# Kernel tuning notes

Hardware: AMD Instinct MI355X
Metric: run time of the kernel (lower is better)

## Reference

```python
import jax, jax.numpy as jnp
import numpy as np

C_S, C_P, FEAT_DIM, NUM_BINS = 256, 128, 64, 22
TOTAL_EDGE_FEATS = FEAT_DIM * 3 + NUM_BINS * 2  # 236
MAX_LEN = 2056


def get_index_embedding(indices, embed_size, max_len=MAX_LEN):
    # indices: [..., ] float; returns [..., embed_size]
    K = jnp.arange(embed_size // 2, dtype=jnp.float32)
    ang = indices[..., None] * jnp.pi / (max_len ** (2.0 * K / embed_size))
    return jnp.concatenate([jnp.sin(ang), jnp.cos(ang)], axis=-1)


def calc_distogram(pos, min_bin, max_bin, num_bins):
    # pos: [B, N, 3] -> one-hot distogram [B, N, N, num_bins]
    d = jnp.linalg.norm(pos[:, :, None, :] - pos[:, None, :, :], axis=-1)[..., None]
    lower = jnp.linspace(min_bin, max_bin, num_bins)
    upper = jnp.concatenate([lower[1:], jnp.array([1e8], dtype=jnp.float32)])
    return ((d > lower) & (d < upper)).astype(pos.dtype)


def layer_norm(x, gamma, beta, eps=1e-5):
    mu = jnp.mean(x, axis=-1, keepdims=True)
    var = jnp.mean((x - mu) ** 2, axis=-1, keepdims=True)
    return (x - mu) * jax.lax.rsqrt(var + eps) * gamma + beta


def setup_inputs() -> dict:
    key = jax.random.key(0)
    ks = jax.random.split(key, 12)
    B, N = 2, 512
    def lin(k, fan_in, shape):
        bound = 1.0 / np.sqrt(fan_in)
        return jax.random.uniform(k, shape, jnp.float32, -bound, bound)
    return {
        "s": jax.random.normal(ks[0], (B, N, C_S), jnp.float32),
        "t": jax.random.normal(ks[1], (B, N, 3), jnp.float32),
        "sc_t": jax.random.normal(ks[2], (B, N, 3), jnp.float32),
        "p_mask": jnp.ones((B, N, N), jnp.float32),
        "W_sp": lin(ks[3], C_S, (FEAT_DIM, C_S)),
        "b_sp": lin(ks[4], C_S, (FEAT_DIM,)),
        "W_rp": lin(ks[5], FEAT_DIM, (FEAT_DIM, FEAT_DIM)),
        "b_rp": lin(ks[5], FEAT_DIM, (FEAT_DIM,)),
        "W1": lin(ks[6], TOTAL_EDGE_FEATS, (C_P, TOTAL_EDGE_FEATS)),
        "b1": lin(ks[7], TOTAL_EDGE_FEATS, (C_P,)),
        "W2": lin(ks[8], C_P, (C_P, C_P)),
        "b2": lin(ks[9], C_P, (C_P,)),
        "W3": lin(ks[10], C_P, (C_P, C_P)),
        "b3": lin(ks[11], C_P, (C_P,)),
        "ln_g": jnp.ones((C_P,), jnp.float32),
        "ln_b": jnp.zeros((C_P,), jnp.float32),
    }


def reference(s, t, sc_t, p_mask, W_sp, b_sp, W_rp, b_rp, W1, b1, W2, b2, W3, b3, ln_g, ln_b):
    B, N, _ = s.shape
    # node embed then all-pairs broadcast-concat: [B,N,N,2*feat_dim]
    p_i = s @ W_sp.T + b_sp  # [B,N,feat_dim]
    cross = jnp.concatenate([
        jnp.broadcast_to(p_i[:, :, None, :], (B, N, N, FEAT_DIM)),
        jnp.broadcast_to(p_i[:, None, :, :], (B, N, N, FEAT_DIM)),
    ], axis=-1)
    # relative position embedding (res_idx=None -> arange)
    pos = jnp.broadcast_to(jnp.arange(N, dtype=jnp.float32)[None, :], (B, N))
    rel_pos = pos[:, :, None] - pos[:, None, :]
    pos_emb = get_index_embedding(rel_pos, FEAT_DIM)  # [B,N,N,feat_dim]
    relpos_feats = pos_emb @ W_rp.T + b_rp
    dist_feats = calc_distogram(t, 1e-3, 20.0, NUM_BINS)
    sc_feats = calc_distogram(sc_t, 1e-3, 20.0, NUM_BINS)
    all_edge = jnp.concatenate([cross, relpos_feats, dist_feats, sc_feats], axis=-1)
    h = jax.nn.relu(all_edge @ W1.T + b1)
    h = jax.nn.relu(h @ W2.T + b2)
    h = h @ W3.T + b3
    h = layer_norm(h, ln_g, ln_b)
    return h * p_mask[..., None]
```

## Files before the change

### kernel.cpp

```cpp
#include <hip/hip_runtime.h>

#define NN 512

typedef __attribute__((ext_vector_type(8))) short bf16x8;
typedef __attribute__((ext_vector_type(4))) float f32x4;

__device__ __forceinline__ unsigned short f2bf(float x) {
    union { float f; unsigned u; } c; c.f = x;
    unsigned u = c.u + 0x7fffu + ((c.u >> 16) & 1u);
    return (unsigned short)(u >> 16);
}

__device__ __forceinline__ float blo(unsigned u) {
    union { unsigned x; float f; } c; c.x = u << 16; return c.f;
}
__device__ __forceinline__ float bhi(unsigned u) {
    union { unsigned x; float f; } c; c.x = u & 0xffff0000u; return c.f;
}

__device__ __forceinline__ unsigned pk2(unsigned a, unsigned b, unsigned c,
                                        unsigned d, unsigned e) {
    float lo = blo(a) + blo(b) + blo(c) + blo(d) + blo(e);
    float hi = bhi(a) + bhi(b) + bhi(c) + bhi(d) + bhi(e);
    lo = fmaxf(lo, 0.0f);
    hi = fmaxf(hi, 0.0f);
    return (unsigned)f2bf(lo) | ((unsigned)f2bf(hi) << 16);
}

__device__ __forceinline__ int find_bin(float d) {
    int bin = 22;
    #pragma unroll
    for (int k = 0; k < 22; ++k) {
        float lo = (float)(1e-3 + k * ((20.0 - 1e-3) / 21.0));
        float hi = (k < 21) ? (float)(1e-3 + (k + 1) * ((20.0 - 1e-3) / 21.0)) : 1e8f;
        if (d > lo && d < hi) bin = k;
    }
    return bin;
}

__global__ __launch_bounds__(128) void k_prep(
        const float* __restrict__ s, const float* __restrict__ t,
        const float* __restrict__ sct,
        const float* __restrict__ Wsp, const float* __restrict__ bsp,
        const float* __restrict__ Wrp, const float* __restrict__ brp,
        const float* __restrict__ W1, const float* __restrict__ b1,
        const float* __restrict__ W2, const float* __restrict__ W3,
        float* __restrict__ p_i, unsigned short* __restrict__ relTb,
        unsigned short* __restrict__ WdTb, unsigned short* __restrict__ WscTb,
        unsigned short* __restrict__ w2a, unsigned short* __restrict__ w3a,
        unsigned short* __restrict__ binT)
{
    __shared__ float sh[2][256];
    const int blk = blockIdx.x, tid = threadIdx.x;

    if (blk < 23) {
        const int bin = blk, c = tid;
        WdTb[bin * 128 + c]  = (bin < 22) ? f2bf(W1[c * 236 + 192 + bin]) : (unsigned short)0;
        WscTb[bin * 128 + c] = (bin < 22) ? f2bf(W1[c * 236 + 214 + bin]) : (unsigned short)0;
    } else if (blk < 55) {
        const int seg = blk - 23;
        const int isW3 = seg >> 4;
        const int idx = (seg & 15) * 128 + tid;
        const int lane = idx & 63, ks = (idx >> 6) & 3, ct = idx >> 8;
        const float* W = isW3 ? W3 : W2;
        unsigned short* dst = isW3 ? w3a : w2a;
        const float* wp = W + (ct * 16 + (lane & 15)) * 128 + ks * 32 + (lane >> 4) * 8;
        unsigned r0 = (unsigned)f2bf(wp[0]) | ((unsigned)f2bf(wp[1]) << 16);
        unsigned r1 = (unsigned)f2bf(wp[2]) | ((unsigned)f2bf(wp[3]) << 16);
        unsigned r2 = (unsigned)f2bf(wp[4]) | ((unsigned)f2bf(wp[5]) << 16);
        unsigned r3 = (unsigned)f2bf(wp[6]) | ((unsigned)f2bf(wp[7]) << 16);
        uint4 v = { r0, r1, r2, r3 };
        *(uint4*)(dst + idx * 8) = v;
    } else if (blk < 1078) {
        const int row = blk - 55;
        const float d = (float)(row - 511);
        if (tid < 32) {
            float f = powf(2056.0f, (float)tid * (1.0f / 32.0f));
            float ang = d * 3.14159265358979323846f / f;
            sh[0][tid] = sinf(ang);
            sh[0][tid + 32] = cosf(ang);
        }
        __syncthreads();
        if (tid < 64) {
            const float* wr = Wrp + tid * 64;
            float a = brp[tid];
            #pragma unroll
            for (int k = 0; k < 64; ++k) a += sh[0][k] * wr[k];
            sh[1][tid] = a;
        }
        __syncthreads();
        const float* w = W1 + tid * 236 + 128;
        float a = b1[tid];
        #pragma unroll
        for (int k = 0; k < 64; ++k) a += sh[1][k] * w[k];
        relTb[row * 128 + tid] = f2bf(a);
    } else if (blk < 1590) {
        const int half = tid >> 6, ch = tid & 63;
        const int row = (blk - 1078) * 2 + half;
        *(float4*)&sh[half][ch * 4] = *(const float4*)&s[row * 256 + ch * 4];
        __syncthreads();
        const float* w = Wsp + ch * 256;
        float acc = bsp[ch];
        #pragma unroll 8
        for (int k = 0; k < 256; k += 4)
            acc += sh[half][k]*w[k] + sh[half][k+1]*w[k+1] + sh[half][k+2]*w[k+2] + sh[half][k+3]*w[k+3];
        p_i[row * 64 + ch] = acc;
    } else {
        const int pair = (blk - 1590) * 128 + tid;
        const int bi = pair >> 9, j = pair & (NN - 1);
        const int rj = (bi & ~(NN - 1)) + j;
        float ax = t[bi*3+0] - t[rj*3+0];
        float ay = t[bi*3+1] - t[rj*3+1];
        float az = t[bi*3+2] - t[rj*3+2];
        int bD = find_bin(sqrtf(ax*ax + ay*ay + az*az));
        float sx = sct[bi*3+0] - sct[rj*3+0];
        float sy = sct[bi*3+1] - sct[rj*3+1];
        float sz = sct[bi*3+2] - sct[rj*3+2];
        int bS = find_bin(sqrtf(sx*sx + sy*sy + sz*sz));
        binT[pair] = (unsigned short)(bD | (bS << 5));
    }
}

__global__ __launch_bounds__(128) void k_ql(const float* __restrict__ p_i,
        const float* __restrict__ W1,
        unsigned short* __restrict__ qLb, unsigned short* __restrict__ qRb)
{
    __shared__ float pr[64];
    const int row = blockIdx.x, tid = threadIdx.x;
    if (tid < 16) *(float4*)&pr[tid * 4] = *(const float4*)&p_i[row * 64 + tid * 4];
    __syncthreads();
    const float* w = W1 + tid * 236;
    float aL = 0.f, aR = 0.f;
    #pragma unroll
    for (int k = 0; k < 64; ++k) { aL += pr[k] * w[k]; aR += pr[k] * w[64 + k]; }
    qLb[row * 128 + tid] = f2bf(aL);
    qRb[row * 128 + tid] = f2bf(aR);
}

#define H1_OFF  0
#define H2_OFF  16384
#define LNP_OFF 32768
#define SMEM_SZ 37888

__global__ __launch_bounds__(512, 4) void k_main(
    const float* __restrict__ pmask,
    const unsigned short* __restrict__ qLb, const unsigned short* __restrict__ qRb,
    const unsigned short* __restrict__ relTb, const unsigned short* __restrict__ WdTb,
    const unsigned short* __restrict__ WscTb, const unsigned short* __restrict__ binT,
    const unsigned short* __restrict__ w2a, const unsigned short* __restrict__ w3a,
    const float* __restrict__ b2, const float* __restrict__ b3,
    const float* __restrict__ lng, const float* __restrict__ lnb,
    float* __restrict__ out)
{
    __shared__ __align__(16) char smem[SMEM_SZ];

    const int tid  = threadIdx.x;
    const int l    = tid & 63;
    const int w    = tid >> 6;
    const int jloc = l & 15;
    const int gq   = l >> 4;

    const int blk   = blockIdx.x;
    const int bi    = blk >> 3;
    const int i     = bi & (NN - 1);
    const int bbase = bi & ~(NN - 1);
    const int j0    = (blk & 7) * 64;

    bf16x8 w2r[4], w3r[4];
    #pragma unroll
    for (int ks = 0; ks < 4; ++ks) {
        w2r[ks] = *(const bf16x8*)(w2a + (w * 256 + ks * 64 + l) * 8);
        w3r[ks] = *(const bf16x8*)(w3a + (w * 256 + ks * 64 + l) * 8);
    }
    const int cch = w * 16 + gq * 4;
    const float4 b2f = *(const float4*)(b2 + cch);
    const float4 b3f = *(const float4*)(b3 + cch);
    const float4 g4  = *(const float4*)(lng + cch);
    const float4 be4 = *(const float4*)(lnb + cch);
    float maskv[4];
    #pragma unroll
    for (int tt = 0; tt < 4; ++tt)
        maskv[tt] = pmask[(size_t)bi * NN + j0 + tt * 16 + jloc];

    {
        const int r = tid >> 3, q = tid & 7;
        const unsigned bv = binT[bi * NN + j0 + r];
        const int bD = bv & 31, bS = (int)(bv >> 5);
        const unsigned short* qLp = qLb + (size_t)bi * 128;
        const unsigned short* qRp = qRb + (size_t)(bbase + j0 + r) * 128;
        const unsigned short* rTp = relTb + (size_t)(i - (j0 + r) + NN - 1) * 128;
        const unsigned short* dTp = WdTb + bD * 128;
        const unsigned short* sTp = WscTb + bS * 128;
        const int hswz = (r & 7) << 4;
        #pragma unroll
        for (int u = 0; u < 2; ++u) {
            const int c0 = q * 16 + u * 8;
            uint4 A = *(const uint4*)(qLp + c0);
            uint4 B = *(const uint4*)(qRp + c0);
            uint4 C = *(const uint4*)(rTp + c0);
            uint4 D = *(const uint4*)(dTp + c0);
            uint4 E = *(const uint4*)(sTp + c0);
            uint4 P;
            P.x = pk2(A.x, B.x, C.x, D.x, E.x);
            P.y = pk2(A.y, B.y, C.y, D.y, E.y);
            P.z = pk2(A.z, B.z, C.z, D.z, E.z);
            P.w = pk2(A.w, B.w, C.w, D.w, E.w);
            *(uint4*)(smem + H1_OFF + ((r * 256 + c0 * 2) ^ hswz)) = P;
        }
    }
    __syncthreads();

    const int rswz = (jloc & 7) << 4;

    #pragma unroll
    for (int tt = 0; tt < 4; ++tt) {
        const int rowb = (tt * 16 + jloc) * 256;
        f32x4 a2 = {0.f, 0.f, 0.f, 0.f};
        #pragma unroll
        for (int ks = 0; ks < 4; ++ks) {
            bf16x8 bfr = *(bf16x8*)(smem + H1_OFF + ((rowb + ks * 64 + gq * 16) ^ rswz));
            a2 = __builtin_amdgcn_mfma_f32_16x16x32_bf16(w2r[ks], bfr, a2, 0, 0, 0);
        }
        float y0 = fmaxf(a2[0] + b2f.x, 0.0f);
        float y1 = fmaxf(a2[1] + b2f.y, 0.0f);
        float y2 = fmaxf(a2[2] + b2f.z, 0.0f);
        float y3 = fmaxf(a2[3] + b2f.w, 0.0f);
        uint2 pk;
        pk.x = (unsigned)f2bf(y0) | ((unsigned)f2bf(y1) << 16);
        pk.y = (unsigned)f2bf(y2) | ((unsigned)f2bf(y3) << 16);
        *(uint2*)(smem + H2_OFF + ((rowb + cch * 2) ^ rswz)) = pk;
    }
    __syncthreads();

    f32x4 acc3[4];
    float* lnp = (float*)(smem + LNP_OFF);
    #pragma unroll
    for (int tt = 0; tt < 4; ++tt) {
        const int rowb = (tt * 16 + jloc) * 256;
        f32x4 a3 = {0.f, 0.f, 0.f, 0.f};
        #pragma unroll
        for (int ks = 0; ks < 4; ++ks) {
            bf16x8 bfr = *(bf16x8*)(smem + H2_OFF + ((rowb + ks * 64 + gq * 16) ^ rswz));
            a3 = __builtin_amdgcn_mfma_f32_16x16x32_bf16(w3r[ks], bfr, a3, 0, 0, 0);
        }
        a3[0] += b3f.x; a3[1] += b3f.y; a3[2] += b3f.z; a3[3] += b3f.w;
        acc3[tt] = a3;
        float s1 = a3[0] + a3[1] + a3[2] + a3[3];
        float s2 = a3[0]*a3[0] + a3[1]*a3[1] + a3[2]*a3[2] + a3[3]*a3[3];
        s1 += __shfl_xor(s1, 16); s2 += __shfl_xor(s2, 16);
        s1 += __shfl_xor(s1, 32); s2 += __shfl_xor(s2, 32);
        if (l < 16) {
            float2 p2 = make_float2(s1, s2);
            *(float2*)(lnp + (tt * 16 + jloc) * 20 + w * 2) = p2;
        }
    }
    __syncthreads();

    #pragma unroll
    for (int tt = 0; tt < 4; ++tt) {
        const int row = tt * 16 + jloc;
        float s1 = 0.f, s2 = 0.f;
        #pragma unroll
        for (int pp = 0; pp < 4; ++pp) {
            float4 v = *(float4*)(lnp + row * 20 + pp * 4);
            s1 += v.x + v.z; s2 += v.y + v.w;
        }
        const float mean = s1 * (1.0f / 128.0f);
        const float var  = s2 * (1.0f / 128.0f) - mean * mean;
        const float rstd = rsqrtf(var + 1e-5f);
        const float mk = maskv[tt];
        f32x4 a3 = acc3[tt];
        f32x4 o;
        o[0] = ((a3[0] - mean) * rstd * g4.x + be4.x) * mk;
        o[1] = ((a3[1] - mean) * rstd * g4.y + be4.y) * mk;
        o[2] = ((a3[2] - mean) * rstd * g4.z + be4.z) * mk;
        o[3] = ((a3[3] - mean) * rstd * g4.w + be4.w) * mk;
        const int slot = (w * 4 + gq) ^ (row & 31);
        *(f32x4*)(smem + row * 512 + slot * 16) = o;
    }
    __syncthreads();

    float* ob = out + ((size_t)(bi * NN + j0)) * 128;
    #pragma unroll
    for (int it = 0; it < 4; ++it) {
        const int boff = it * 8192 + tid * 16;
        const int row  = boff >> 9;
        const int slot = (boff >> 4) & 31;
        const int sslt = slot ^ (row & 31);
        f32x4 v = *(f32x4*)(smem + row * 512 + sslt * 16);
        __builtin_nontemporal_store(v, (f32x4*)(ob + (boff >> 2)));
    }
}

extern "C" void kernel_launch(void* const* d_in, const int* in_sizes, int n_in,
                              void* d_out, int out_size, void* d_ws, size_t ws_size,
                              hipStream_t stream)
{
    const float* s   = (const float*)d_in[0];
    const float* t   = (const float*)d_in[1];
    const float* sct = (const float*)d_in[2];
    const float* pm  = (const float*)d_in[3];
    const float* Wsp = (const float*)d_in[4];
    const float* bsp = (const float*)d_in[5];
    const float* Wrp = (const float*)d_in[6];
    const float* brp = (const float*)d_in[7];
    const float* W1  = (const float*)d_in[8];
    const float* b1  = (const float*)d_in[9];
    const float* W2  = (const float*)d_in[10];
    const float* b2  = (const float*)d_in[11];
    const float* W3  = (const float*)d_in[12];
    const float* b3  = (const float*)d_in[13];
    const float* lng = (const float*)d_in[14];
    const float* lnb = (const float*)d_in[15];

    float* ws = (float*)d_ws;
    float*          p_i   = ws;
    unsigned short* qLb   = (unsigned short*)(ws + 65536);
    unsigned short* qRb   = (unsigned short*)(ws + 131072);
    unsigned short* relTb = (unsigned short*)(ws + 196608);
    unsigned short* WdTb  = (unsigned short*)(ws + 262144);
    unsigned short* WscTb = (unsigned short*)(ws + 263616);
    unsigned short* w2a   = (unsigned short*)(ws + 265088);
    unsigned short* w3a   = (unsigned short*)(ws + 273280);
    unsigned short* binT  = (unsigned short*)(ws + 281472);

    k_prep<<<5686, 128, 0, stream>>>(s, t, sct, Wsp, bsp, Wrp, brp, W1, b1, W2, W3,
                                     p_i, relTb, WdTb, WscTb, w2a, w3a, binT);
    k_ql<<<1024, 128, 0, stream>>>(p_i, W1, qLb, qRb);
    k_main<<<8192, 512, 0, stream>>>(pm, qLb, qRb, relTb, WdTb, WscTb, binT,
                                     w2a, w3a, b2, b3, lng, lnb, (float*)d_out);
}
```

Measured before the change: 128.4 us.

## Retile MLP MFMA work as 2x4 wave grid with 2 column tiles per wave

Each wave now owns 32 rows by 32 output channels, a 2x4 grid over the 64x128 tile, instead of 16 channels across all 64 rows. Each B-fragment read from shared memory feeds two MFMAs, which halves LDS reads for layers 2 and 3. The LayerNorm partial-sum buffer shrinks to 4 partials per row. The cost is twice the weight registers per wave (16 bf16x8 vectors), which may raise register pressure at 512 threads and 4 blocks per SM. Bias and gamma/beta are now loaded inside the loops rather than hoisted.

Measured after the change: 131.4 us. 2.3% more time.

```diff
diff --git a/kernel.cpp b/kernel.cpp
--- a/kernel.cpp
+++ b/kernel.cpp
@@ -140,7 +140,7 @@
 #define H1_OFF  0
 #define H2_OFF  16384
 #define LNP_OFF 32768
-#define SMEM_SZ 37888
+#define SMEM_SZ 35840
 
 __global__ __launch_bounds__(512, 4) void k_main(
     const float* __restrict__ pmask,
@@ -157,6 +157,8 @@
     const int tid  = threadIdx.x;
     const int l    = tid & 63;
     const int w    = tid >> 6;
+    const int wr   = w >> 2;
+    const int wc   = w & 3;
     const int jloc = l & 15;
     const int gq   = l >> 4;
 
@@ -166,21 +168,19 @@
     const int bbase = bi & ~(NN - 1);
     const int j0    = (blk & 7) * 64;
 
-    bf16x8 w2r[4], w3r[4];
-    #pragma unroll
-    for (int ks = 0; ks < 4; ++ks) {
-        w2r[ks] = *(const bf16x8*)(w2a + (w * 256 + ks * 64 + l) * 8);
-        w3r[ks] = *(const bf16x8*)(w3a + (w * 256 + ks * 64 + l) * 8);
-    }
-    const int cch = w * 16 + gq * 4;
-    const float4 b2f = *(const float4*)(b2 + cch);
-    const float4 b3f = *(const float4*)(b3 + cch);
-    const float4 g4  = *(const float4*)(lng + cch);
-    const float4 be4 = *(const float4*)(lnb + cch);
-    float maskv[4];
-    #pragma unroll
-    for (int tt = 0; tt < 4; ++tt)
-        maskv[tt] = pmask[(size_t)bi * NN + j0 + tt * 16 + jloc];
+    bf16x8 w2r[2][4], w3r[2][4];
+    #pragma unroll
+    for (int cc = 0; cc < 2; ++cc)
+        #pragma unroll
+        for (int ks = 0; ks < 4; ++ks) {
+            const int fi = ((wc * 2 + cc) * 256 + ks * 64 + l) * 8;
+            w2r[cc][ks] = *(const bf16x8*)(w2a + fi);
+            w3r[cc][ks] = *(const bf16x8*)(w3a + fi);
+        }
+    float maskv[2];
+    #pragma unroll
+    for (int rt = 0; rt < 2; ++rt)
+        maskv[rt] = pmask[(size_t)bi * NN + j0 + wr * 32 + rt * 16 + jloc];
 
     {
         const int r = tid >> 3, q = tid & 7;
@@ -213,70 +213,88 @@
     const int rswz = (jloc & 7) << 4;
 
     #pragma unroll
-    for (int tt = 0; tt < 4; ++tt) {
-        const int rowb = (tt * 16 + jloc) * 256;
-        f32x4 a2 = {0.f, 0.f, 0.f, 0.f};
+    for (int rt = 0; rt < 2; ++rt) {
+        const int rowb = (wr * 32 + rt * 16 + jloc) * 256;
+        f32x4 a2[2] = { {0.f,0.f,0.f,0.f}, {0.f,0.f,0.f,0.f} };
         #pragma unroll
         for (int ks = 0; ks < 4; ++ks) {
             bf16x8 bfr = *(bf16x8*)(smem + H1_OFF + ((rowb + ks * 64 + gq * 16) ^ rswz));
-            a2 = __builtin_amdgcn_mfma_f32_16x16x32_bf16(w2r[ks], bfr, a2, 0, 0, 0);
-        }
-        float y0 = fmaxf(a2[0] + b2f.x, 0.0f);
-        float y1 = fmaxf(a2[1] + b2f.y, 0.0f);
-        float y2 = fmaxf(a2[2] + b2f.z, 0.0f);
-        float y3 = fmaxf(a2[3] + b2f.w, 0.0f);
-        uint2 pk;
-        pk.x = (unsigned)f2bf(y0) | ((unsigned)f2bf(y1) << 16);
-        pk.y = (unsigned)f2bf(y2) | ((unsigned)f2bf(y3) << 16);
-        *(uint2*)(smem + H2_OFF + ((rowb + cch * 2) ^ rswz)) = pk;
-    }
-    __syncthreads();
-
-    f32x4 acc3[4];
+            a2[0] = __builtin_amdgcn_mfma_f32_16x16x32_bf16(w2r[0][ks], bfr, a2[0], 0, 0, 0);
+            a2[1] = __builtin_amdgcn_mfma_f32_16x16x32_bf16(w2r[1][ks], bfr, a2[1], 0, 0, 0);
+        }
+        #pragma unroll
+        for (int cc = 0; cc < 2; ++cc) {
+            const int c = wc * 32 + cc * 16 + gq * 4;
+            float4 bb = *(const float4*)(b2 + c);
+            float y0 = fmaxf(a2[cc][0] + bb.x, 0.0f);
+            float y1 = fmaxf(a2[cc][1] + bb.y, 0.0f);
+            float y2 = fmaxf(a2[cc][2] + bb.z, 0.0f);
+            float y3 = fmaxf(a2[cc][3] + bb.w, 0.0f);
+            uint2 pk;
+            pk.x = (unsigned)f2bf(y0) | ((unsigned)f2bf(y1) << 16);
+            pk.y = (unsigned)f2bf(y2) | ((unsigned)f2bf(y3) << 16);
+            *(uint2*)(smem + H2_OFF + ((rowb + c * 2) ^ rswz)) = pk;
+        }
+    }
+    __syncthreads();
+
+    f32x4 acc3[2][2];
     float* lnp = (float*)(smem + LNP_OFF);
     #pragma unroll
-    for (int tt = 0; tt < 4; ++tt) {
-        const int rowb = (tt * 16 + jloc) * 256;
-        f32x4 a3 = {0.f, 0.f, 0.f, 0.f};
+    for (int rt = 0; rt < 2; ++rt) {
+        const int rowb = (wr * 32 + rt * 16 + jloc) * 256;
+        f32x4 a3[2] = { {0.f,0.f,0.f,0.f}, {0.f,0.f,0.f,0.f} };
         #pragma unroll
         for (int ks = 0; ks < 4; ++ks) {
             bf16x8 bfr = *(bf16x8*)(smem + H2_OFF + ((rowb + ks * 64 + gq * 16) ^ rswz));
-            a3 = __builtin_amdgcn_mfma_f32_16x16x32_bf16(w3r[ks], bfr, a3, 0, 0, 0);
-        }
-        a3[0] += b3f.x; a3[1] += b3f.y; a3[2] += b3f.z; a3[3] += b3f.w;
-        acc3[tt] = a3;
-        float s1 = a3[0] + a3[1] + a3[2] + a3[3];
-        float s2 = a3[0]*a3[0] + a3[1]*a3[1] + a3[2]*a3[2] + a3[3]*a3[3];
+            a3[0] = __builtin_amdgcn_mfma_f32_16x16x32_bf16(w3r[0][ks], bfr, a3[0], 0, 0, 0);
+            a3[1] = __builtin_amdgcn_mfma_f32_16x16x32_bf16(w3r[1][ks], bfr, a3[1], 0, 0, 0);
+        }
+        float s1 = 0.f, s2 = 0.f;
+        #pragma unroll
+        for (int cc = 0; cc < 2; ++cc) {
+            const int c = wc * 32 + cc * 16 + gq * 4;
+            float4 bb = *(const float4*)(b3 + c);
+            a3[cc][0] += bb.x; a3[cc][1] += bb.y;
+            a3[cc][2] += bb.z; a3[cc][3] += bb.w;
+            acc3[cc][rt] = a3[cc];
+            #pragma unroll
+            for (int r = 0; r < 4; ++r) { float v = a3[cc][r]; s1 += v; s2 += v * v; }
+        }
         s1 += __shfl_xor(s1, 16); s2 += __shfl_xor(s2, 16);
         s1 += __shfl_xor(s1, 32); s2 += __shfl_xor(s2, 32);
         if (l < 16) {
-            float2 p2 = make_float2(s1, s2);
-            *(float2*)(lnp + (tt * 16 + jloc) * 20 + w * 2) = p2;
-        }
-    }
-    __syncthreads();
-
-    #pragma unroll
-    for (int tt = 0; tt < 4; ++tt) {
-        const int row = tt * 16 + jloc;
-        float s1 = 0.f, s2 = 0.f;
-        #pragma unroll
-        for (int pp = 0; pp < 4; ++pp) {
-            float4 v = *(float4*)(lnp + row * 20 + pp * 4);
-            s1 += v.x + v.z; s2 += v.y + v.w;
-        }
+            const int row = wr * 32 + rt * 16 + jloc;
+            *(float2*)(lnp + row * 12 + wc * 2) = make_float2(s1, s2);
+        }
+    }
+    __syncthreads();
+
+    #pragma unroll
+    for (int rt = 0; rt < 2; ++rt) {
+        const int row = wr * 32 + rt * 16 + jloc;
+        float4 v0 = *(float4*)(lnp + row * 12);
+        float4 v1 = *(float4*)(lnp + row * 12 + 4);
+        const float s1 = v0.x + v0.z + v1.x + v1.z;
+        const float s2 = v0.y + v0.w + v1.y + v1.w;
         const float mean = s1 * (1.0f / 128.0f);
         const float var  = s2 * (1.0f / 128.0f) - mean * mean;
         const float rstd = rsqrtf(var + 1e-5f);
-        const float mk = maskv[tt];
-        f32x4 a3 = acc3[tt];
-        f32x4 o;
-        o[0] = ((a3[0] - mean) * rstd * g4.x + be4.x) * mk;
-        o[1] = ((a3[1] - mean) * rstd * g4.y + be4.y) * mk;
-        o[2] = ((a3[2] - mean) * rstd * g4.z + be4.z) * mk;
-        o[3] = ((a3[3] - mean) * rstd * g4.w + be4.w) * mk;
-        const int slot = (w * 4 + gq) ^ (row & 31);
-        *(f32x4*)(smem + row * 512 + slot * 16) = o;
+        const float mk = maskv[rt];
+        #pragma unroll
+        for (int cc = 0; cc < 2; ++cc) {
+            const int c = wc * 32 + cc * 16 + gq * 4;
+            float4 g4  = *(const float4*)(lng + c);
+            float4 be4 = *(const float4*)(lnb + c);
+            f32x4 a3 = acc3[cc][rt];
+            f32x4 o;
+            o[0] = ((a3[0] - mean) * rstd * g4.x + be4.x) * mk;
+            o[1] = ((a3[1] - mean) * rstd * g4.y + be4.y) * mk;
+            o[2] = ((a3[2] - mean) * rstd * g4.z + be4.z) * mk;
+            o[3] = ((a3[3] - mean) * rstd * g4.w + be4.w) * mk;
+            const int slot = (wc * 8 + cc * 4 + gq) ^ (row & 31);
+            *(f32x4*)(smem + row * 512 + slot * 16) = o;
+        }
     }
     __syncthreads();
 
```
